# Kernel tuning notes

Hardware: AMD Instinct MI355X
Metric: run time of the kernel (lower is better)

The kernel has to match this reference:

```python
import jax, jax.numpy as jnp
import numpy as np

# Module hyperparameters (from init_kwargs)
DEPTH = 4
SMOOTH_STEP_PARAM = 1.0
TREES_NUM = 16
INPUT_DIM = 2048
OUTPUT_DIM = 512
BATCH = 8192
NUM_LEAVES = 2 ** DEPTH          # 16
NUM_INTERNAL = NUM_LEAVES - 1    # 15


def _routing_matrix():
    """R[n, l] = +1 if leaf l is in the left subtree of node n (gate = s),
    -1 if in the right subtree (gate = 1 - s), 0 if node n not on leaf l's path.
    Node indexing: root = 0, children of n are 2n+1 (left), 2n+2 (right)."""
    R = np.zeros((NUM_INTERNAL, NUM_LEAVES), dtype=np.float32)
    for l in range(NUM_LEAVES):
        node = 0
        for lvl in range(DEPTH):
            bit = (l >> (DEPTH - 1 - lvl)) & 1  # 0 = go left, 1 = go right
            R[node, l] = 1.0 if bit == 0 else -1.0
            node = 2 * node + 1 + bit
    return R

ROUTE = jnp.asarray(_routing_matrix())  # [NUM_INTERNAL, NUM_LEAVES]


def smooth_step(v):
    # TEL smooth-step: t = clip(ssp * v + 0.5, 0, 1); s = -2t^3 + 3t^2
    t = jnp.clip(SMOOTH_STEP_PARAM * v + 0.5, 0.0, 1.0)
    return t * t * (3.0 - 2.0 * t)


def setup_inputs() -> dict:
    key = jax.random.key(0)
    k1, k2, k3 = jax.random.split(key, 3)
    x = jax.random.normal(k1, (BATCH, INPUT_DIM), dtype=jnp.float32)
    node_weights = jax.random.normal(k2, (TREES_NUM, INPUT_DIM, NUM_INTERNAL), dtype=jnp.float32) * 0.02
    leaf_weights = jax.random.normal(k3, (TREES_NUM, OUTPUT_DIM, NUM_LEAVES), dtype=jnp.float32) * 0.02
    return {"x": x, "node_weights": node_weights, "leaf_weights": leaf_weights}


def reference(x, node_weights, leaf_weights):
    # Node pre-activations for all trees: [B, T, NUM_INTERNAL]
    a = jnp.einsum('bi,tin->btn', x, node_weights)
    s = smooth_step(a)  # probability of routing LEFT at each internal node
    left = (ROUTE == 1.0)
    right = (ROUTE == -1.0)
    # Per-(node, leaf) routing factor; nodes off the path contribute 1.
    terms = jnp.where(left, s[..., None], jnp.where(right, 1.0 - s[..., None], 1.0))  # [B,T,NI,NL]
    leaf_prob = jnp.prod(terms, axis=2)  # [B, T, NUM_LEAVES]
    # Weighted leaf aggregation, summed over trees (sum_outputs=True)
    out = jnp.einsum('btl,tol->bo', leaf_prob, leaf_weights)  # [B, OUTPUT_DIM]
    return out
```

## Files before the change

kernel.cpp:

```cpp
#include <hip/hip_runtime.h>
#include <cstdint>
#include <cstddef>

typedef __fp16 half8 __attribute__((ext_vector_type(8)));
typedef float  f32x4 __attribute__((ext_vector_type(4)));

#define BATCH 8192
#define INDIM 2048
#define OUTD  512
#define NC    256
#define BM    32
#define BK    128
#define NCH   (INDIM / BK)

__device__ __forceinline__ half8 cvt8(float4 a, float4 b) {
  half8 h;
  h[0] = (__fp16)a.x; h[1] = (__fp16)a.y; h[2] = (__fp16)a.z; h[3] = (__fp16)a.w;
  h[4] = (__fp16)b.x; h[5] = (__fp16)b.y; h[6] = (__fp16)b.z; h[7] = (__fp16)b.w;
  return h;
}

__global__ __launch_bounds__(256)
void kprepW(const float* __restrict__ nw, __fp16* __restrict__ WrT) {
  __shared__ float Ls[128][16];
  const int tid = threadIdx.x;
  const int t  = blockIdx.x >> 4;
  const int k0 = (blockIdx.x & 15) * 128;
  const float* base = nw + ((size_t)t * INDIM + k0) * 15;
  #pragma unroll
  for (int i = 0; i < 8; i++) {
    int fl = tid + 256 * i;
    if (fl < 1920) {
      float v = base[fl];
      int kk = (int)(((unsigned)fl * 8739u) >> 17);
      int n  = fl - 15 * kk;
      Ls[kk][n] = v;
    }
  }
  __syncthreads();
  const int n  = tid >> 4;
  const int kc = tid & 15;
  half8 h = {};
  if (n < 15) {
    #pragma unroll
    for (int j = 0; j < 8; j++) h[j] = (__fp16)Ls[kc * 8 + j][n];
  }
  *(half8*)(WrT + (size_t)(16 * t + n) * INDIM + k0 + kc * 8) = h;
}

__global__ __launch_bounds__(256)
void kprepL(const float* __restrict__ lw, __fp16* __restrict__ LWrT) {
  int g = blockIdx.x * 256 + threadIdx.x;
  int o = g >> 4;
  int t = g & 15;
  const float* src = lw + ((size_t)t * OUTD + o) * 16;
  float4 a = *(const float4*)(src);
  float4 b = *(const float4*)(src + 4);
  float4 c = *(const float4*)(src + 8);
  float4 d = *(const float4*)(src + 12);
  *(half8*)(LWrT + (size_t)o * NC + t * 16)     = cvt8(a, b);
  *(half8*)(LWrT + (size_t)o * NC + t * 16 + 8) = cvt8(c, d);
}

__global__ __launch_bounds__(512, 1)
void kfused(const float* __restrict__ x, const __fp16* __restrict__ WrT,
            const __fp16* __restrict__ LWrT, float* __restrict__ out) {
  __shared__ char   uni[BM * NC * 4];
  __shared__ __fp16 Ps[BM * NC];
  __fp16* Xs = (__fp16*)uni;
  float*  As = (float*)uni;

  const int tid  = threadIdx.x;
  const int lane = tid & 63;
  const int wv   = tid >> 6;
  const int l15  = lane & 15;
  const int lg   = lane >> 4;
  const int r0   = blockIdx.x * BM;
  const int sr   = tid >> 4;
  const int sk   = tid & 15;
  const int sOff = (sr * BK + sk * 8) ^ ((sr & 7) << 3);

  const float* xrow = x + (size_t)(r0 + sr) * INDIM + sk * 8;
  const __fp16* wbase = WrT + (size_t)(32 * wv + l15) * INDIM + lg * 8;

  f32x4 acc1[2][2] = {};

  half8 bfA[2][4], bfB[2][4];
  float4 xN0, xN1, xM0, xM1;

  #define LDB(dst, ch)                                                          \
    _Pragma("unroll") for (int nt = 0; nt < 2; nt++)                            \
    _Pragma("unroll") for (int ks = 0; ks < 4; ks++)                            \
      dst[nt][ks] = *(const half8*)(wbase + (size_t)nt * 16 * INDIM + (ch) * BK + ks * 32);

  #define LDX(d0, d1, ch)                                                       \
    d0 = *(const float4*)(xrow + (ch) * BK);                                    \
    d1 = *(const float4*)(xrow + (ch) * BK + 4);

  #define STX(buf, d0, d1)                                                      \
    *(half8*)&Xs[(buf) * (BM * BK) + sOff] = cvt8(d0, d1);

  #define COMPUTE(buf, bf)                                                      \
    _Pragma("unroll") for (int ks = 0; ks < 4; ks++) {                          \
      half8 af[2];                                                              \
      _Pragma("unroll") for (int mt = 0; mt < 2; mt++) {                        \
        const int r = l15 + 16 * mt;                                            \
        const int e = (r * BK + ks * 32 + lg * 8) ^ ((r & 7) << 3);             \
        af[mt] = *(const half8*)&Xs[(buf) * (BM * BK) + e];                     \
      }                                                                         \
      _Pragma("unroll") for (int mt = 0; mt < 2; mt++)                          \
      _Pragma("unroll") for (int nt = 0; nt < 2; nt++)                          \
        acc1[mt][nt] = __builtin_amdgcn_mfma_f32_16x16x32_f16(af[mt], bf[nt][ks], acc1[mt][nt], 0, 0, 0); \
    }

  { float4 a, b; LDX(a, b, 0); STX(0, a, b); }
  LDX(xN0, xN1, 1);
  LDB(bfA, 0);

  #pragma unroll 1
  for (int ch = 0; ch < NCH; ch += 2) {
    LDB(bfB, ch + 1);
    if (ch + 2 < NCH) { LDX(xM0, xM1, ch + 2); }
    __syncthreads();
    STX(1, xN0, xN1);
    COMPUTE(0, bfA);
    if (ch + 2 < NCH) { LDB(bfA, ch + 2); }
    if (ch + 3 < NCH) { LDX(xN0, xN1, ch + 3); }
    __syncthreads();
    if (ch + 2 < NCH) { STX(0, xM0, xM1); }
    COMPUTE(1, bfB);
  }

  __syncthreads();

  #pragma unroll
  for (int mt = 0; mt < 2; mt++)
    #pragma unroll
    for (int nt = 0; nt < 2; nt++)
      #pragma unroll
      for (int i = 0; i < 4; i++)
        As[(16 * mt + 4 * lg + i) * NC + 32 * wv + 16 * nt + l15] = acc1[mt][nt][i];
  __syncthreads();

  {
    const int row = tid >> 4, tr = tid & 15;
    float av[16];
    #pragma unroll
    for (int q = 0; q < 4; q++) {
      f32x4 v = *(const f32x4*)&As[row * NC + tr * 16 + 4 * q];
      av[4 * q + 0] = v[0]; av[4 * q + 1] = v[1];
      av[4 * q + 2] = v[2]; av[4 * q + 3] = v[3];
    }
    float sg[15];
    #pragma unroll
    for (int m = 0; m < 15; m++) {
      float t = fminf(fmaxf(av[m] + 0.5f, 0.f), 1.f);
      sg[m] = t * t * (3.f - 2.f * t);
    }
    float p[16];
    #pragma unroll
    for (int l = 0; l < 16; l++) {
      float pr = 1.f; int node = 0;
      #pragma unroll
      for (int L = 0; L < 4; L++) {
        int bit = (l >> (3 - L)) & 1;
        pr *= bit ? (1.f - sg[node]) : sg[node];
        node = 2 * node + 1 + bit;
      }
      p[l] = pr;
    }
    half8 h0, h1;
    #pragma unroll
    for (int j = 0; j < 8; j++) { h0[j] = (__fp16)p[j]; h1[j] = (__fp16)p[8 + j]; }
    const int base = row * NC + tr * 16;
    const int swz  = (row & 7) << 3;
    *(half8*)&Ps[(base) ^ swz]     = h0;
    *(half8*)&Ps[(base + 8) ^ swz] = h1;
  }
  __syncthreads();

  f32x4 acc2[2][4] = {};
  const __fp16* lbase = LWrT + (size_t)(64 * wv + l15) * NC + lg * 8;
  #pragma unroll
  for (int kc = 0; kc < 2; kc++) {
    half8 bf2[4][4];
    #pragma unroll
    for (int nt = 0; nt < 4; nt++)
      #pragma unroll
      for (int ks = 0; ks < 4; ks++)
        bf2[nt][ks] = *(const half8*)(lbase + (size_t)nt * 16 * NC + kc * 128 + ks * 32);
    #pragma unroll
    for (int ks = 0; ks < 4; ks++) {
      half8 af[2];
      #pragma unroll
      for (int mt = 0; mt < 2; mt++) {
        const int r = l15 + 16 * mt;
        const int e = (r * NC + kc * 128 + ks * 32 + lg * 8) ^ ((r & 7) << 3);
        af[mt] = *(const half8*)&Ps[e];
      }
      #pragma unroll
      for (int mt = 0; mt < 2; mt++)
        #pragma unroll
        for (int nt = 0; nt < 4; nt++)
          acc2[mt][nt] = __builtin_amdgcn_mfma_f32_16x16x32_f16(af[mt], bf2[nt][ks], acc2[mt][nt], 0, 0, 0);
    }
  }
  #pragma unroll
  for (int mt = 0; mt < 2; mt++)
    #pragma unroll
    for (int nt = 0; nt < 4; nt++)
      #pragma unroll
      for (int i = 0; i < 4; i++)
        out[(size_t)(r0 + 16 * mt + 4 * lg + i) * OUTD + 64 * wv + 16 * nt + l15] = acc2[mt][nt][i];
}

extern "C" void kernel_launch(void* const* d_in, const int* in_sizes, int n_in,
                              void* d_out, int out_size, void* d_ws, size_t ws_size,
                              hipStream_t stream) {
  const float* x  = (const float*)d_in[0];
  const float* nw = (const float*)d_in[1];
  const float* lw = (const float*)d_in[2];
  float* out = (float*)d_out;

  __fp16* WrT  = (__fp16*)d_ws;
  __fp16* LWrT = (__fp16*)((char*)d_ws + (size_t)NC * INDIM * 2);

  hipLaunchKernelGGL(kprepW, dim3(256), dim3(256), 0, stream, nw, WrT);
  hipLaunchKernelGGL(kprepL, dim3(32),  dim3(256), 0, stream, lw, LWrT);
  hipLaunchKernelGGL(kfused, dim3(BATCH / BM), dim3(512), 0, stream, x, WrT, LWrT, out);
}
```

Baseline: 137.1 us.

## Restructure GEMM1 pipeline with larger K chunk and coalesced leaf-weight prep

Doubles the K chunk of the first GEMM so each barrier covers twice the work, and replaces the two-chunk register prefetch of weight fragments with per-k-step loads straight from global memory. The x chunk is still prefetched into registers and double-buffered in LDS with a single barrier per iteration. The leaf-weight prep kernel now stages through shared memory, so reads are coalesced and the transposed fp16 writes are contiguous, and it runs on more blocks. Loading the weight fragments inside the inner loop risks exposing global latency that the old explicit prefetch hid.

```diff
diff --git a/kernel.cpp b/kernel.cpp
--- a/kernel.cpp
+++ b/kernel.cpp
@@ -10,7 +10,7 @@
 #define OUTD  512
 #define NC    256
 #define BM    32
-#define BK    128
+#define BK    256
 #define NCH   (INDIM / BK)
 
 __device__ __forceinline__ half8 cvt8(float4 a, float4 b) {
@@ -50,16 +50,23 @@
 
 __global__ __launch_bounds__(256)
 void kprepL(const float* __restrict__ lw, __fp16* __restrict__ LWrT) {
-  int g = blockIdx.x * 256 + threadIdx.x;
-  int o = g >> 4;
-  int t = g & 15;
-  const float* src = lw + ((size_t)t * OUTD + o) * 16;
-  float4 a = *(const float4*)(src);
-  float4 b = *(const float4*)(src + 4);
-  float4 c = *(const float4*)(src + 8);
-  float4 d = *(const float4*)(src + 12);
-  *(half8*)(LWrT + (size_t)o * NC + t * 16)     = cvt8(a, b);
-  *(half8*)(LWrT + (size_t)o * NC + t * 16 + 8) = cvt8(c, d);
+  __shared__ float Ls[128][17];
+  const int tid = threadIdx.x;
+  const int t  = blockIdx.x >> 2;
+  const int o0 = (blockIdx.x & 3) * 128;
+  const float* base = lw + ((size_t)t * OUTD + o0) * 16;
+  #pragma unroll
+  for (int i = 0; i < 8; i++) {
+    int fl = tid + 256 * i;
+    Ls[fl >> 4][fl & 15] = base[fl];
+  }
+  __syncthreads();
+  const int ol = tid >> 1;
+  const int h  = tid & 1;
+  half8 v;
+  #pragma unroll
+  for (int j = 0; j < 8; j++) v[j] = (__fp16)Ls[ol][8 * h + j];
+  *(half8*)(LWrT + (size_t)(o0 + ol) * NC + 16 * t + 8 * h) = v;
 }
 
 __global__ __launch_bounds__(512, 1)
@@ -77,61 +84,58 @@
   const int lg   = lane >> 4;
   const int r0   = blockIdx.x * BM;
   const int sr   = tid >> 4;
-  const int sk   = tid & 15;
-  const int sOff = (sr * BK + sk * 8) ^ ((sr & 7) << 3);
-
-  const float* xrow = x + (size_t)(r0 + sr) * INDIM + sk * 8;
+  const int seg  = tid & 15;
+
+  const float*  xrow  = x + (size_t)(r0 + sr) * INDIM + seg * 16;
   const __fp16* wbase = WrT + (size_t)(32 * wv + l15) * INDIM + lg * 8;
 
+  const int sE0 = (sr * BK + seg * 16)     ^ ((sr & 7) << 3);
+  const int sE1 = (sr * BK + seg * 16 + 8) ^ ((sr & 7) << 3);
+
   f32x4 acc1[2][2] = {};
-
-  half8 bfA[2][4], bfB[2][4];
-  float4 xN0, xN1, xM0, xM1;
-
-  #define LDB(dst, ch)                                                          \
-    _Pragma("unroll") for (int nt = 0; nt < 2; nt++)                            \
-    _Pragma("unroll") for (int ks = 0; ks < 4; ks++)                            \
-      dst[nt][ks] = *(const half8*)(wbase + (size_t)nt * 16 * INDIM + (ch) * BK + ks * 32);
-
-  #define LDX(d0, d1, ch)                                                       \
-    d0 = *(const float4*)(xrow + (ch) * BK);                                    \
-    d1 = *(const float4*)(xrow + (ch) * BK + 4);
-
-  #define STX(buf, d0, d1)                                                      \
-    *(half8*)&Xs[(buf) * (BM * BK) + sOff] = cvt8(d0, d1);
-
-  #define COMPUTE(buf, bf)                                                      \
-    _Pragma("unroll") for (int ks = 0; ks < 4; ks++) {                          \
-      half8 af[2];                                                              \
-      _Pragma("unroll") for (int mt = 0; mt < 2; mt++) {                        \
-        const int r = l15 + 16 * mt;                                            \
-        const int e = (r * BK + ks * 32 + lg * 8) ^ ((r & 7) << 3);             \
-        af[mt] = *(const half8*)&Xs[(buf) * (BM * BK) + e];                     \
-      }                                                                         \
-      _Pragma("unroll") for (int mt = 0; mt < 2; mt++)                          \
-      _Pragma("unroll") for (int nt = 0; nt < 2; nt++)                          \
-        acc1[mt][nt] = __builtin_amdgcn_mfma_f32_16x16x32_f16(af[mt], bf[nt][ks], acc1[mt][nt], 0, 0, 0); \
-    }
-
-  { float4 a, b; LDX(a, b, 0); STX(0, a, b); }
-  LDX(xN0, xN1, 1);
-  LDB(bfA, 0);
+  float4 px[4];
+
+  {
+    const float* p = xrow;
+    float4 a0 = *(const float4*)(p);      float4 a1 = *(const float4*)(p + 4);
+    float4 a2 = *(const float4*)(p + 8);  float4 a3 = *(const float4*)(p + 12);
+    *(half8*)&Xs[sE0] = cvt8(a0, a1);
+    *(half8*)&Xs[sE1] = cvt8(a2, a3);
+  }
+  __syncthreads();
 
   #pragma unroll 1
-  for (int ch = 0; ch < NCH; ch += 2) {
-    LDB(bfB, ch + 1);
-    if (ch + 2 < NCH) { LDX(xM0, xM1, ch + 2); }
+  for (int ch = 0; ch < NCH; ++ch) {
+    const int cur = ch & 1;
+    const bool more = (ch + 1 < NCH);
+    if (more) {
+      const float* p = xrow + (ch + 1) * BK;
+      px[0] = *(const float4*)(p);      px[1] = *(const float4*)(p + 4);
+      px[2] = *(const float4*)(p + 8);  px[3] = *(const float4*)(p + 12);
+    }
+    #pragma unroll
+    for (int ks = 0; ks < BK / 32; ks++) {
+      half8 bf0 = *(const half8*)(wbase + (size_t)0  * INDIM + ch * BK + ks * 32);
+      half8 bf1 = *(const half8*)(wbase + (size_t)16 * INDIM + ch * BK + ks * 32);
+      half8 af[2];
+      #pragma unroll
+      for (int mt = 0; mt < 2; mt++) {
+        const int r = l15 + 16 * mt;
+        const int e = (r * BK + ks * 32 + lg * 8) ^ ((r & 7) << 3);
+        af[mt] = *(const half8*)&Xs[cur * (BM * BK) + e];
+      }
+      acc1[0][0] = __builtin_amdgcn_mfma_f32_16x16x32_f16(af[0], bf0, acc1[0][0], 0, 0, 0);
+      acc1[0][1] = __builtin_amdgcn_mfma_f32_16x16x32_f16(af[0], bf1, acc1[0][1], 0, 0, 0);
+      acc1[1][0] = __builtin_amdgcn_mfma_f32_16x16x32_f16(af[1], bf0, acc1[1][0], 0, 0, 0);
+      acc1[1][1] = __builtin_amdgcn_mfma_f32_16x16x32_f16(af[1], bf1, acc1[1][1], 0, 0, 0);
+    }
+    if (more) {
+      const int off = (cur ^ 1) * (BM * BK);
+      *(half8*)&Xs[off + sE0] = cvt8(px[0], px[1]);
+      *(half8*)&Xs[off + sE1] = cvt8(px[2], px[3]);
+    }
     __syncthreads();
-    STX(1, xN0, xN1);
-    COMPUTE(0, bfA);
-    if (ch + 2 < NCH) { LDB(bfA, ch + 2); }
-    if (ch + 3 < NCH) { LDX(xN0, xN1, ch + 3); }
-    __syncthreads();
-    if (ch + 2 < NCH) { STX(0, xM0, xM1); }
-    COMPUTE(1, bfB);
-  }
-
-  __syncthreads();
+  }
 
   #pragma unroll
   for (int mt = 0; mt < 2; mt++)
@@ -226,6 +230,6 @@
   __fp16* LWrT = (__fp16*)((char*)d_ws + (size_t)NC * INDIM * 2);
 
   hipLaunchKernelGGL(kprepW, dim3(256), dim3(256), 0, stream, nw, WrT);
-  hipLaunchKernelGGL(kprepL, dim3(32),  dim3(256), 0, stream, lw, LWrT);
+  hipLaunchKernelGGL(kprepL, dim3(64),  dim3(256), 0, stream, lw, LWrT);
   hipLaunchKernelGGL(kfused, dim3(BATCH / BM), dim3(512), 0, stream, x, WrT, LWrT, out);
 }
```

New measurement: 146.7 us. 1.07x slower.
